# Optimization experiments

Measured on AMD Instinct MI355X. Metric: run time of the kernel, lower is better.

Reference implementation:

```python
import jax, jax.numpy as jnp
import numpy as np

B, H, M, D, MID, DV = 128, 8, 196, 128, 64, 128


def setup_inputs() -> dict:
    key0 = jax.random.key(0)
    ks = jax.random.split(key0, 12)
    query = jax.random.normal(ks[0], (B, H, D), dtype=jnp.float32)
    key = jax.random.normal(ks[1], (B, H, M, D), dtype=jnp.float32)
    att_mask = jax.random.randint(ks[2], (B, M), 0, 2).astype(jnp.float32)
    att_mask = att_mask.at[:, 0].set(1.0)  # guarantee each row has >=1 valid slot
    value1 = jax.random.normal(ks[3], (B, H, DV), dtype=jnp.float32)
    value2 = jax.random.normal(ks[4], (B, H, M, DV), dtype=jnp.float32)
    W_basic = jax.random.normal(ks[5], (D, MID), dtype=jnp.float32) * 0.05
    b_basic = jnp.zeros((MID,), dtype=jnp.float32)
    W_spatial = jax.random.normal(ks[6], (MID, 1), dtype=jnp.float32) * 0.05
    b_spatial = jnp.zeros((1,), dtype=jnp.float32)
    W_channel = jax.random.normal(ks[7], (MID, DV), dtype=jnp.float32) * 0.05
    b_channel = jnp.zeros((DV,), dtype=jnp.float32)
    return {
        'query': query, 'key': key, 'att_mask': att_mask,
        'value1': value1, 'value2': value2,
        'W_basic': W_basic, 'b_basic': b_basic,
        'W_spatial': W_spatial, 'b_spatial': b_spatial,
        'W_channel': W_channel, 'b_channel': b_channel,
    }


def reference(query, key, att_mask, value1, value2,
              W_basic, b_basic, W_spatial, b_spatial, W_channel, b_channel):
    # att_map: broadcast elementwise QK product  [B,H,M,D]
    att_map = query[..., None, :] * key
    # attention_basic: Linear + ReLU (Dropout is identity at eval)  [B,H,M,MID]
    h = jax.nn.relu(jnp.einsum('bhmd,de->bhme', att_map, W_basic) + b_basic)
    # masked mean-pool over regions  [B,H,MID]
    mask_ext = att_mask[:, None, :, None]  # [B,1,M,1]
    att_map_pool = jnp.sum(h * mask_ext, axis=-2) / jnp.sum(mask_ext, axis=-2)
    # spatial attention logits  [B,H,M]
    alpha_spatial = (jnp.einsum('bhme,eo->bhmo', h, W_spatial) + b_spatial)[..., 0]
    alpha_spatial = jnp.where(att_mask[:, None, :] == 0, -1e9, alpha_spatial)
    alpha_spatial = jax.nn.softmax(alpha_spatial, axis=-1)
    # weighted sum over regions  [B,H,DV]
    v2 = jnp.einsum('bhm,bhmv->bhv', alpha_spatial, value2)
    # channel gate  [B,H,DV]
    alpha_channel = jax.nn.sigmoid(jnp.einsum('bhe,ev->bhv', att_map_pool, W_channel) + b_channel)
    return value1 * v2 * alpha_channel
```

## Files before the change

### kernel.cpp

```cpp
#include <hip/hip_runtime.h>
#include <cstddef>

#define NBH  1024
#define Mm   196
#define Dd   128
#define MIDe 64
#define DVv  128
#define WQLD 136

typedef __attribute__((ext_vector_type(8))) short bf16x8;
typedef __attribute__((ext_vector_type(4))) float f32x4;

__device__ __forceinline__ short f2bf(float x) {
    union { float f; unsigned u; } v; v.f = x;
    return (short)((v.u + 0x7FFFu + ((v.u >> 16) & 1u)) >> 16);
}

__device__ __forceinline__ float waveReduceSum(float v) {
#pragma unroll
    for (int off = 32; off > 0; off >>= 1) v += __shfl_xor(v, off, 64);
    return v;
}

__device__ __forceinline__ float waveReduceMax(float v) {
#pragma unroll
    for (int off = 32; off > 0; off >>= 1) v = fmaxf(v, __shfl_xor(v, off, 64));
    return v;
}

__global__ __launch_bounds__(256, 4)
void scatt_fused(const float* __restrict__ query,
                 const float* __restrict__ key,
                 const float* __restrict__ att_mask,
                 const float* __restrict__ value1,
                 const float* __restrict__ value2,
                 const float* __restrict__ W_basic,
                 const float* __restrict__ b_basic,
                 const float* __restrict__ W_spatial,
                 const float* __restrict__ b_spatial,
                 const float* __restrict__ W_channel,
                 const float* __restrict__ b_channel,
                 float* __restrict__ out)
{
    __shared__ short wqT[MIDe][WQLD];
    __shared__ float qS[Dd];
    __shared__ float maskS[Mm];
    __shared__ float sS[Mm];
    __shared__ float poolPart[4][MIDe];
    __shared__ float poolS[MIDe];
    __shared__ float partS[8][DVv];
    __shared__ float redS[12];

    const int t    = threadIdx.x;
    const int lane = t & 63;
    const int w    = t >> 6;
    const int ln15 = lane & 15;
    const int q4   = lane >> 4;
    const int bh   = blockIdx.x;
    const int b    = bh >> 3;

    const float* __restrict__ keyB  = key      + (size_t)bh * Mm * Dd;
    const float* __restrict__ val2B = value2   + (size_t)bh * Mm * DVv;
    const float* __restrict__ qB    = query    + (size_t)bh * Dd;
    const float* __restrict__ maskB = att_mask + (size_t)b  * Mm;

    if (t < 32) ((float4*)qS)[t] = ((const float4*)qB)[t];
    for (int i = t; i < Mm; i += 256) maskS[i] = maskB[i];
    __syncthreads();

    {
        const int e0 = lane;
        const int d0 = w * 32;
#pragma unroll
        for (int c = 0; c < 4; ++c) {
            short pk[8];
#pragma unroll
            for (int j = 0; j < 8; ++j) {
                const int d = d0 + c * 8 + j;
                pk[j] = f2bf(qS[d] * W_basic[d * MIDe + e0]);
            }
            *(bf16x8*)&wqT[e0][d0 + c * 8] = *(bf16x8*)pk;
        }
    }
    __syncthreads();

    bf16x8 bfr[4][4];
#pragma unroll
    for (int ks = 0; ks < 4; ++ks)
#pragma unroll
        for (int nt = 0; nt < 4; ++nt)
            bfr[ks][nt] = *(const bf16x8*)&wqT[nt * 16 + ln15][ks * 32 + q4 * 8];

    float bbv[4], wspv[4];
#pragma unroll
    for (int nt = 0; nt < 4; ++nt) {
        bbv[nt]  = b_basic[nt * 16 + ln15];
        wspv[nt] = W_spatial[nt * 16 + ln15];
    }
    const float bsp = b_spatial[0];
    float poolAcc[4] = {0.f, 0.f, 0.f, 0.f};

    for (int mt = w; mt < 13; mt += 4) {
        const int mrow = min(mt * 16 + ln15, Mm - 1);
        const float* ap = keyB + (size_t)mrow * Dd + q4 * 8;
        float4 a0[4], a1[4];
#pragma unroll
        for (int ks = 0; ks < 4; ++ks) {
            a0[ks] = *(const float4*)(ap + ks * 32);
            a1[ks] = *(const float4*)(ap + ks * 32 + 4);
        }
        f32x4 acc[4] = {f32x4{0,0,0,0}, f32x4{0,0,0,0},
                        f32x4{0,0,0,0}, f32x4{0,0,0,0}};
#pragma unroll
        for (int ks = 0; ks < 4; ++ks) {
            const bf16x8 af = { f2bf(a0[ks].x), f2bf(a0[ks].y),
                                f2bf(a0[ks].z), f2bf(a0[ks].w),
                                f2bf(a1[ks].x), f2bf(a1[ks].y),
                                f2bf(a1[ks].z), f2bf(a1[ks].w) };
#pragma unroll
            for (int nt = 0; nt < 4; ++nt)
                acc[nt] = __builtin_amdgcn_mfma_f32_16x16x32_bf16(
                              af, bfr[ks][nt], acc[nt], 0, 0, 0);
        }
#pragma unroll
        for (int r = 0; r < 4; ++r) {
            const int m = mt * 16 + q4 * 4 + r;
            const bool valid = m < Mm;
            const float msk = valid ? maskS[m] : 0.f;
            float srow = 0.f;
#pragma unroll
            for (int nt = 0; nt < 4; ++nt) {
                float hv = acc[nt][r] + bbv[nt];
                hv = hv > 0.f ? hv : 0.f;
                poolAcc[nt] = fmaf(hv, msk, poolAcc[nt]);
                srow = fmaf(hv, wspv[nt], srow);
            }
            srow += __shfl_xor(srow, 1, 64);
            srow += __shfl_xor(srow, 2, 64);
            srow += __shfl_xor(srow, 4, 64);
            srow += __shfl_xor(srow, 8, 64);
            if (valid && ln15 == 0) sS[m] = srow + bsp;
        }
    }
#pragma unroll
    for (int nt = 0; nt < 4; ++nt) {
        poolAcc[nt] += __shfl_xor(poolAcc[nt], 16, 64);
        poolAcc[nt] += __shfl_xor(poolAcc[nt], 32, 64);
    }
    if (lane < 16) {
#pragma unroll
        for (int nt = 0; nt < 4; ++nt)
            poolPart[w][nt * 16 + lane] = poolAcc[nt];
    }
    __syncthreads();

    const float myMask = (t < Mm) ? maskS[t] : 0.f;
    float myS = -3.0e38f;
    if (t < Mm) {
        myS = sS[t];
        if (myMask == 0.f) myS = -1.0e9f;
    }
    const float rmx = waveReduceMax(myS);
    if (lane == 0) redS[w] = rmx;
    __syncthreads();
    const float mx = fmaxf(fmaxf(redS[0], redS[1]), fmaxf(redS[2], redS[3]));
    const float ev = (t < Mm) ? __expf(myS - mx) : 0.f;
    const float s1 = waveReduceSum(ev);
    const float s2 = waveReduceSum(myMask);
    if (lane == 0) { redS[4 + w] = s1; redS[8 + w] = s2; }
    __syncthreads();
    const float denom = redS[4] + redS[5] + redS[6] + redS[7];
    const float cnt   = redS[8] + redS[9] + redS[10] + redS[11];
    if (t < Mm) sS[t] = ev / denom;
    if (t < MIDe)
        poolS[t] = (poolPart[0][t] + poolPart[1][t] + poolPart[2][t] + poolPart[3][t]) / cnt;
    __syncthreads();

    float chv = 0.f;
    if (t < DVv) {
        float a = b_channel[t];
#pragma unroll 8
        for (int e = 0; e < MIDe; ++e)
            a = fmaf(poolS[e], W_channel[e * DVv + t], a);
        chv = 1.f / (1.f + __expf(-a));
    }

    const int vq = t & 31;
    const int ms = t >> 5;
    float4 acc4 = make_float4(0.f, 0.f, 0.f, 0.f);
#pragma unroll 5
    for (int m = ms; m < Mm; m += 8) {
        const float a = sS[m];
        const float4 vv = *(const float4*)(val2B + (size_t)m * DVv + 4 * vq);
        acc4.x = fmaf(a, vv.x, acc4.x);
        acc4.y = fmaf(a, vv.y, acc4.y);
        acc4.z = fmaf(a, vv.z, acc4.z);
        acc4.w = fmaf(a, vv.w, acc4.w);
    }
    ((float4*)&partS[ms][0])[vq] = acc4;
    __syncthreads();

    if (t < DVv) {
        float v2v = 0.f;
#pragma unroll
        for (int i = 0; i < 8; ++i) v2v += partS[i][t];
        out[(size_t)bh * DVv + t] = value1[(size_t)bh * DVv + t] * v2v * chv;
    }
}

extern "C" void kernel_launch(void* const* d_in, const int* in_sizes, int n_in,
                              void* d_out, int out_size, void* d_ws, size_t ws_size,
                              hipStream_t stream) {
    const float* query     = (const float*)d_in[0];
    const float* key       = (const float*)d_in[1];
    const float* att_mask  = (const float*)d_in[2];
    const float* value1    = (const float*)d_in[3];
    const float* value2    = (const float*)d_in[4];
    const float* W_basic   = (const float*)d_in[5];
    const float* b_basic   = (const float*)d_in[6];
    const float* W_spatial = (const float*)d_in[7];
    const float* b_spatial = (const float*)d_in[8];
    const float* W_channel = (const float*)d_in[9];
    const float* b_channel = (const float*)d_in[10];
    float* out = (float*)d_out;

    scatt_fused<<<NBH, 256, 0, stream>>>(query, key, att_mask, value1, value2,
                                         W_basic, b_basic, W_spatial, b_spatial,
                                         W_channel, b_channel, out);
}
```

Before: 243.9 us.

## Split fused kernel into three kernels with per-tile GEMM grid

```diff
diff --git a/kernel.cpp b/kernel.cpp
--- a/kernel.cpp
+++ b/kernel.cpp
@@ -6,10 +6,15 @@
 #define Dd   128
 #define MIDe 64
 #define DVv  128
-#define WQLD 136
+#define NMT  13
+#define SLD  208
 
 typedef __attribute__((ext_vector_type(8))) short bf16x8;
 typedef __attribute__((ext_vector_type(4))) float f32x4;
+
+#define WQ_SHORTS   ((size_t)NBH * 16 * 64 * 8)
+#define SW_FLOATS   ((size_t)NBH * SLD)
+#define POOL_FLOATS ((size_t)NBH * NMT * 64)
 
 __device__ __forceinline__ short f2bf(float x) {
     union { float f; unsigned u; } v; v.f = x;
@@ -28,28 +33,13 @@
     return v;
 }
 
-__global__ __launch_bounds__(256, 4)
-void scatt_fused(const float* __restrict__ query,
-                 const float* __restrict__ key,
-                 const float* __restrict__ att_mask,
-                 const float* __restrict__ value1,
-                 const float* __restrict__ value2,
-                 const float* __restrict__ W_basic,
-                 const float* __restrict__ b_basic,
-                 const float* __restrict__ W_spatial,
-                 const float* __restrict__ b_spatial,
-                 const float* __restrict__ W_channel,
-                 const float* __restrict__ b_channel,
-                 float* __restrict__ out)
+__global__ __launch_bounds__(256)
+void build_wq(const float* __restrict__ query,
+              const float* __restrict__ W_basic,
+              short* __restrict__ wqF)
 {
-    __shared__ short wqT[MIDe][WQLD];
     __shared__ float qS[Dd];
-    __shared__ float maskS[Mm];
-    __shared__ float sS[Mm];
-    __shared__ float poolPart[4][MIDe];
-    __shared__ float poolS[MIDe];
-    __shared__ float partS[8][DVv];
-    __shared__ float redS[12];
+    __shared__ short wqT[MIDe][136];
 
     const int t    = threadIdx.x;
     const int lane = t & 63;
@@ -57,20 +47,12 @@
     const int ln15 = lane & 15;
     const int q4   = lane >> 4;
     const int bh   = blockIdx.x;
-    const int b    = bh >> 3;
-
-    const float* __restrict__ keyB  = key      + (size_t)bh * Mm * Dd;
-    const float* __restrict__ val2B = value2   + (size_t)bh * Mm * DVv;
-    const float* __restrict__ qB    = query    + (size_t)bh * Dd;
-    const float* __restrict__ maskB = att_mask + (size_t)b  * Mm;
-
-    if (t < 32) ((float4*)qS)[t] = ((const float4*)qB)[t];
-    for (int i = t; i < Mm; i += 256) maskS[i] = maskB[i];
+
+    if (t < 32) ((float4*)qS)[t] = ((const float4*)(query + (size_t)bh * Dd))[t];
     __syncthreads();
 
     {
-        const int e0 = lane;
-        const int d0 = w * 32;
+        const int e0 = lane, d0 = w * 32;
 #pragma unroll
         for (int c = 0; c < 4; ++c) {
             short pk[8];
@@ -84,12 +66,44 @@
     }
     __syncthreads();
 
-    bf16x8 bfr[4][4];
-#pragma unroll
-    for (int ks = 0; ks < 4; ++ks)
-#pragma unroll
-        for (int nt = 0; nt < 4; ++nt)
-            bfr[ks][nt] = *(const bf16x8*)&wqT[nt * 16 + ln15][ks * 32 + q4 * 8];
+    short* dst = wqF + ((size_t)bh * 16 + w * 4) * 512 + lane * 8;
+#pragma unroll
+    for (int nt = 0; nt < 4; ++nt) {
+        const bf16x8 f = *(const bf16x8*)&wqT[nt * 16 + ln15][w * 32 + q4 * 8];
+        *(bf16x8*)(dst + nt * 512) = f;
+    }
+}
+
+__global__ __launch_bounds__(64, 3)
+void gemm_tile(const float* __restrict__ key,
+               const float* __restrict__ att_mask,
+               const float* __restrict__ b_basic,
+               const float* __restrict__ W_spatial,
+               const float* __restrict__ b_spatial,
+               const short* __restrict__ wqF,
+               float* __restrict__ sW,
+               float* __restrict__ poolW)
+{
+    const int lane = threadIdx.x;
+    const int ln15 = lane & 15;
+    const int q4   = lane >> 4;
+    const int mt   = blockIdx.x;
+    const int bh   = blockIdx.y;
+    const int b    = bh >> 3;
+
+    const int mrow = min(mt * 16 + ln15, Mm - 1);
+    const float* ap = key + ((size_t)bh * Mm + mrow) * Dd + q4 * 8;
+    float4 a0[4], a1[4];
+#pragma unroll
+    for (int ks = 0; ks < 4; ++ks) {
+        a0[ks] = *(const float4*)(ap + ks * 32);
+        a1[ks] = *(const float4*)(ap + ks * 32 + 4);
+    }
+    const short* wp = wqF + (size_t)bh * 8192 + lane * 8;
+    bf16x8 bfr[16];
+#pragma unroll
+    for (int i = 0; i < 16; ++i)
+        bfr[i] = *(const bf16x8*)(wp + (size_t)i * 512);
 
     float bbv[4], wspv[4];
 #pragma unroll
@@ -98,49 +112,40 @@
         wspv[nt] = W_spatial[nt * 16 + ln15];
     }
     const float bsp = b_spatial[0];
+
+    f32x4 acc[4] = {f32x4{0,0,0,0}, f32x4{0,0,0,0},
+                    f32x4{0,0,0,0}, f32x4{0,0,0,0}};
+#pragma unroll
+    for (int ks = 0; ks < 4; ++ks) {
+        const bf16x8 af = { f2bf(a0[ks].x), f2bf(a0[ks].y),
+                            f2bf(a0[ks].z), f2bf(a0[ks].w),
+                            f2bf(a1[ks].x), f2bf(a1[ks].y),
+                            f2bf(a1[ks].z), f2bf(a1[ks].w) };
+#pragma unroll
+        for (int nt = 0; nt < 4; ++nt)
+            acc[nt] = __builtin_amdgcn_mfma_f32_16x16x32_bf16(
+                          af, bfr[ks * 4 + nt], acc[nt], 0, 0, 0);
+    }
+
     float poolAcc[4] = {0.f, 0.f, 0.f, 0.f};
-
-    for (int mt = w; mt < 13; mt += 4) {
-        const int mrow = min(mt * 16 + ln15, Mm - 1);
-        const float* ap = keyB + (size_t)mrow * Dd + q4 * 8;
-        float4 a0[4], a1[4];
-#pragma unroll
-        for (int ks = 0; ks < 4; ++ks) {
-            a0[ks] = *(const float4*)(ap + ks * 32);
-            a1[ks] = *(const float4*)(ap + ks * 32 + 4);
+#pragma unroll
+    for (int r = 0; r < 4; ++r) {
+        const int m = mt * 16 + q4 * 4 + r;
+        const bool valid = m < Mm;
+        const float msk = valid ? att_mask[b * Mm + m] : 0.f;
+        float srow = 0.f;
+#pragma unroll
+        for (int nt = 0; nt < 4; ++nt) {
+            float hv = acc[nt][r] + bbv[nt];
+            hv = hv > 0.f ? hv : 0.f;
+            poolAcc[nt] = fmaf(hv, msk, poolAcc[nt]);
+            srow = fmaf(hv, wspv[nt], srow);
         }
-        f32x4 acc[4] = {f32x4{0,0,0,0}, f32x4{0,0,0,0},
-                        f32x4{0,0,0,0}, f32x4{0,0,0,0}};
-#pragma unroll
-        for (int ks = 0; ks < 4; ++ks) {
-            const bf16x8 af = { f2bf(a0[ks].x), f2bf(a0[ks].y),
-                                f2bf(a0[ks].z), f2bf(a0[ks].w),
-                                f2bf(a1[ks].x), f2bf(a1[ks].y),
-                                f2bf(a1[ks].z), f2bf(a1[ks].w) };
-#pragma unroll
-            for (int nt = 0; nt < 4; ++nt)
-                acc[nt] = __builtin_amdgcn_mfma_f32_16x16x32_bf16(
-                              af, bfr[ks][nt], acc[nt], 0, 0, 0);
-        }
-#pragma unroll
-        for (int r = 0; r < 4; ++r) {
-            const int m = mt * 16 + q4 * 4 + r;
-            const bool valid = m < Mm;
-            const float msk = valid ? maskS[m] : 0.f;
-            float srow = 0.f;
-#pragma unroll
-            for (int nt = 0; nt < 4; ++nt) {
-                float hv = acc[nt][r] + bbv[nt];
-                hv = hv > 0.f ? hv : 0.f;
-                poolAcc[nt] = fmaf(hv, msk, poolAcc[nt]);
-                srow = fmaf(hv, wspv[nt], srow);
-            }
-            srow += __shfl_xor(srow, 1, 64);
-            srow += __shfl_xor(srow, 2, 64);
-            srow += __shfl_xor(srow, 4, 64);
-            srow += __shfl_xor(srow, 8, 64);
-            if (valid && ln15 == 0) sS[m] = srow + bsp;
-        }
+        srow += __shfl_xor(srow, 1, 64);
+        srow += __shfl_xor(srow, 2, 64);
+        srow += __shfl_xor(srow, 4, 64);
+        srow += __shfl_xor(srow, 8, 64);
+        if (valid && ln15 == 0) sW[(size_t)bh * SLD + m] = srow + bsp;
     }
 #pragma unroll
     for (int nt = 0; nt < 4; ++nt) {
@@ -150,14 +155,37 @@
     if (lane < 16) {
 #pragma unroll
         for (int nt = 0; nt < 4; ++nt)
-            poolPart[w][nt * 16 + lane] = poolAcc[nt];
-    }
-    __syncthreads();
-
-    const float myMask = (t < Mm) ? maskS[t] : 0.f;
+            poolW[(size_t)bh * (NMT * 64) + mt * 64 + nt * 16 + lane] = poolAcc[nt];
+    }
+}
+
+__global__ __launch_bounds__(256)
+void finish(const float* __restrict__ att_mask,
+            const float* __restrict__ value1,
+            const float* __restrict__ value2,
+            const float* __restrict__ W_channel,
+            const float* __restrict__ b_channel,
+            const float* __restrict__ sW,
+            const float* __restrict__ poolW,
+            float* __restrict__ out)
+{
+    __shared__ float sS[Mm];
+    __shared__ float poolS[MIDe];
+    __shared__ float partS[8][DVv];
+    __shared__ float redS[12];
+
+    const int t    = threadIdx.x;
+    const int lane = t & 63;
+    const int w    = t >> 6;
+    const int bh   = blockIdx.x;
+    const int b    = bh >> 3;
+
+    const float* __restrict__ val2B = value2 + (size_t)bh * Mm * DVv;
+
+    const float myMask = (t < Mm) ? att_mask[b * Mm + t] : 0.f;
     float myS = -3.0e38f;
     if (t < Mm) {
-        myS = sS[t];
+        myS = sW[(size_t)bh * SLD + t];
         if (myMask == 0.f) myS = -1.0e9f;
     }
     const float rmx = waveReduceMax(myS);
@@ -172,14 +200,19 @@
     const float denom = redS[4] + redS[5] + redS[6] + redS[7];
     const float cnt   = redS[8] + redS[9] + redS[10] + redS[11];
     if (t < Mm) sS[t] = ev / denom;
-    if (t < MIDe)
-        poolS[t] = (poolPart[0][t] + poolPart[1][t] + poolPart[2][t] + poolPart[3][t]) / cnt;
+    if (t < MIDe) {
+        float p = 0.f;
+#pragma unroll
+        for (int mt = 0; mt < NMT; ++mt)
+            p += poolW[(size_t)bh * (NMT * 64) + mt * 64 + t];
+        poolS[t] = p / cnt;
+    }
     __syncthreads();
 
     float chv = 0.f;
     if (t < DVv) {
         float a = b_channel[t];
-#pragma unroll 8
+#pragma unroll 16
         for (int e = 0; e < MIDe; ++e)
             a = fmaf(poolS[e], W_channel[e * DVv + t], a);
         chv = 1.f / (1.f + __expf(-a));
@@ -188,14 +221,17 @@
     const int vq = t & 31;
     const int ms = t >> 5;
     float4 acc4 = make_float4(0.f, 0.f, 0.f, 0.f);
-#pragma unroll 5
-    for (int m = ms; m < Mm; m += 8) {
-        const float a = sS[m];
-        const float4 vv = *(const float4*)(val2B + (size_t)m * DVv + 4 * vq);
-        acc4.x = fmaf(a, vv.x, acc4.x);
-        acc4.y = fmaf(a, vv.y, acc4.y);
-        acc4.z = fmaf(a, vv.z, acc4.z);
-        acc4.w = fmaf(a, vv.w, acc4.w);
+#pragma unroll
+    for (int i = 0; i < 25; ++i) {
+        const int m = ms + 8 * i;
+        if (m < Mm) {
+            const float a = sS[m];
+            const float4 vv = *(const float4*)(val2B + (size_t)m * DVv + 4 * vq);
+            acc4.x = fmaf(a, vv.x, acc4.x);
+            acc4.y = fmaf(a, vv.y, acc4.y);
+            acc4.z = fmaf(a, vv.z, acc4.z);
+            acc4.w = fmaf(a, vv.w, acc4.w);
+        }
     }
     ((float4*)&partS[ms][0])[vq] = acc4;
     __syncthreads();
@@ -224,7 +260,14 @@
     const float* b_channel = (const float*)d_in[10];
     float* out = (float*)d_out;
 
-    scatt_fused<<<NBH, 256, 0, stream>>>(query, key, att_mask, value1, value2,
-                                         W_basic, b_basic, W_spatial, b_spatial,
-                                         W_channel, b_channel, out);
-}
+    short* wqF  = (short*)d_ws;
+    float* sW   = (float*)((char*)d_ws + WQ_SHORTS * sizeof(short));
+    float* poolW = sW + SW_FLOATS;
+
+    build_wq<<<NBH, 256, 0, stream>>>(query, W_basic, wqF);
+    gemm_tile<<<dim3(NMT, NBH), 64, 0, stream>>>(key, att_mask, b_basic,
+                                                 W_spatial, b_spatial,
+                                                 wqF, sW, poolW);
+    finish<<<NBH, 256, 0, stream>>>(att_mask, value1, value2, W_channel,
+                                    b_channel, sW, poolW, out);
+}
```

Result: slower. 260.0 us (+6.6%).

## Prefetch next key tile in registers and read weight fragments from LDS per MFMA

Applied to the files above, without the earlier changes.

```diff
diff --git a/kernel.cpp b/kernel.cpp
--- a/kernel.cpp
+++ b/kernel.cpp
@@ -6,7 +6,6 @@
 #define Dd   128
 #define MIDe 64
 #define DVv  128
-#define WQLD 136
 
 typedef __attribute__((ext_vector_type(8))) short bf16x8;
 typedef __attribute__((ext_vector_type(4))) float f32x4;
@@ -28,7 +27,7 @@
     return v;
 }
 
-__global__ __launch_bounds__(256, 4)
+__global__ __launch_bounds__(256, 3)
 void scatt_fused(const float* __restrict__ query,
                  const float* __restrict__ key,
                  const float* __restrict__ att_mask,
@@ -42,7 +41,7 @@
                  const float* __restrict__ b_channel,
                  float* __restrict__ out)
 {
-    __shared__ short wqT[MIDe][WQLD];
+    __shared__ short wqT[MIDe][136];
     __shared__ float qS[Dd];
     __shared__ float maskS[Mm];
     __shared__ float sS[Mm];
@@ -69,8 +68,7 @@
     __syncthreads();
 
     {
-        const int e0 = lane;
-        const int d0 = w * 32;
+        const int e0 = lane, d0 = w * 32;
 #pragma unroll
         for (int c = 0; c < 4; ++c) {
             short pk[8];
@@ -82,14 +80,6 @@
             *(bf16x8*)&wqT[e0][d0 + c * 8] = *(bf16x8*)pk;
         }
     }
-    __syncthreads();
-
-    bf16x8 bfr[4][4];
-#pragma unroll
-    for (int ks = 0; ks < 4; ++ks)
-#pragma unroll
-        for (int nt = 0; nt < 4; ++nt)
-            bfr[ks][nt] = *(const bf16x8*)&wqT[nt * 16 + ln15][ks * 32 + q4 * 8];
 
     float bbv[4], wspv[4];
 #pragma unroll
@@ -100,15 +90,25 @@
     const float bsp = b_spatial[0];
     float poolAcc[4] = {0.f, 0.f, 0.f, 0.f};
 
+    auto loadA = [&](int mt_, float4* x0, float4* x1) {
+        const int mrow = min(mt_ * 16 + ln15, Mm - 1);
+        const float* ap = keyB + (size_t)mrow * Dd + q4 * 8;
+#pragma unroll
+        for (int ks = 0; ks < 4; ++ks) {
+            x0[ks] = *(const float4*)(ap + ks * 32);
+            x1[ks] = *(const float4*)(ap + ks * 32 + 4);
+        }
+    };
+
+    float4 a0[4], a1[4];
+    loadA(w, a0, a1);
+    __syncthreads();
+
     for (int mt = w; mt < 13; mt += 4) {
-        const int mrow = min(mt * 16 + ln15, Mm - 1);
-        const float* ap = keyB + (size_t)mrow * Dd + q4 * 8;
-        float4 a0[4], a1[4];
-#pragma unroll
-        for (int ks = 0; ks < 4; ++ks) {
-            a0[ks] = *(const float4*)(ap + ks * 32);
-            a1[ks] = *(const float4*)(ap + ks * 32 + 4);
-        }
+        float4 n0[4], n1[4];
+        const int mtn = mt + 4;
+        if (mtn < 13) loadA(mtn, n0, n1);
+
         f32x4 acc[4] = {f32x4{0,0,0,0}, f32x4{0,0,0,0},
                         f32x4{0,0,0,0}, f32x4{0,0,0,0}};
 #pragma unroll
@@ -118,10 +118,14 @@
                                 f2bf(a1[ks].x), f2bf(a1[ks].y),
                                 f2bf(a1[ks].z), f2bf(a1[ks].w) };
 #pragma unroll
-            for (int nt = 0; nt < 4; ++nt)
+            for (int nt = 0; nt < 4; ++nt) {
+                const bf16x8 bf =
+                    *(const bf16x8*)&wqT[nt * 16 + ln15][ks * 32 + q4 * 8];
                 acc[nt] = __builtin_amdgcn_mfma_f32_16x16x32_bf16(
-                              af, bfr[ks][nt], acc[nt], 0, 0, 0);
-        }
+                              af, bf, acc[nt], 0, 0, 0);
+            }
+        }
+
 #pragma unroll
         for (int r = 0; r < 4; ++r) {
             const int m = mt * 16 + q4 * 4 + r;
@@ -141,6 +145,8 @@
             srow += __shfl_xor(srow, 8, 64);
             if (valid && ln15 == 0) sS[m] = srow + bsp;
         }
+#pragma unroll
+        for (int ks = 0; ks < 4; ++ks) { a0[ks] = n0[ks]; a1[ks] = n1[ks]; }
     }
 #pragma unroll
     for (int nt = 0; nt < 4; ++nt) {
@@ -179,7 +185,7 @@
     float chv = 0.f;
     if (t < DVv) {
         float a = b_channel[t];
-#pragma unroll 8
+#pragma unroll 16
         for (int e = 0; e < MIDe; ++e)
             a = fmaf(poolS[e], W_channel[e * DVv + t], a);
         chv = 1.f / (1.f + __expf(-a));
@@ -188,14 +194,17 @@
     const int vq = t & 31;
     const int ms = t >> 5;
     float4 acc4 = make_float4(0.f, 0.f, 0.f, 0.f);
-#pragma unroll 5
-    for (int m = ms; m < Mm; m += 8) {
-        const float a = sS[m];
-        const float4 vv = *(const float4*)(val2B + (size_t)m * DVv + 4 * vq);
-        acc4.x = fmaf(a, vv.x, acc4.x);
-        acc4.y = fmaf(a, vv.y, acc4.y);
-        acc4.z = fmaf(a, vv.z, acc4.z);
-        acc4.w = fmaf(a, vv.w, acc4.w);
+#pragma unroll
+    for (int i = 0; i < 25; ++i) {
+        const int m = ms + 8 * i;
+        if (m < Mm) {
+            const float a = sS[m];
+            const float4 vv = *(const float4*)(val2B + (size_t)m * DVv + 4 * vq);
+            acc4.x = fmaf(a, vv.x, acc4.x);
+            acc4.y = fmaf(a, vv.y, acc4.y);
+            acc4.z = fmaf(a, vv.z, acc4.z);
+            acc4.w = fmaf(a, vv.w, acc4.w);
+        }
     }
     ((float4*)&partS[ms][0])[vq] = acc4;
     __syncthreads();
```

New measurement: 246.7 us. About the same (+1.1%).
